# Kernel optimization log

Measured on AMD Instinct MI355X. Metric: run time of the kernel, lower is better.

## Reference

```python
import jax, jax.numpy as jnp
import numpy as np

DIM = 16  # size_in
N = 16384  # batch of samples


def _g_single(x, W1, b1, W2, b2):
    # myLinear forward for one sample x: [dim] -> [dim*dim] (symmetrized)
    h = jnp.tanh(W1 @ x + b1)                    # [dim]
    out = (W2 @ h + b2).reshape(DIM, DIM)        # [dim, dim]
    out = out + out.T                            # symmetrize (out + out.permute(0,2,1))
    return out.reshape(DIM * DIM)


def setup_inputs() -> dict:
    key = jax.random.key(0)
    k0, k1, k2, k3, k4 = jax.random.split(key, 5)
    s1 = 1.0 / np.sqrt(DIM)   # nn.Linear default init bound for fan_in=dim
    inp = jax.random.normal(k0, (N, 2 * DIM), dtype=jnp.float32)
    W1 = jax.random.uniform(k1, (DIM, DIM), dtype=jnp.float32, minval=-s1, maxval=s1)
    b1 = jax.random.uniform(k2, (DIM,), dtype=jnp.float32, minval=-s1, maxval=s1)
    W2 = jax.random.uniform(k3, (DIM * DIM, DIM), dtype=jnp.float32, minval=-s1, maxval=s1)
    b2 = jax.random.uniform(k4, (DIM * DIM,), dtype=jnp.float32, minval=-s1, maxval=s1)
    return {"t": 0, "input_": inp, "W1": W1, "b1": b1, "W2": W2, "b2": b2}


def reference(t, input_, W1, b1, W2, b2):
    x = input_[:, :DIM]   # [N, dim]
    v = input_[:, DIM:]   # [N, dim]

    g_fn = lambda xx: _g_single(xx, W1, b1, W2, b2)

    # batch jacobian of g w.r.t. x: [N, dim*dim, dim] -> [N, dim, dim, dim]
    J = jax.vmap(jax.jacfwd(g_fn))(x).reshape(N, DIM, DIM, DIM)
    g = jax.vmap(g_fn)(x).reshape(N, DIM, DIM)   # metric, symmetric
    g_inv = jnp.linalg.inv(g)                    # batched small inverse

    # faithful to the source: 4-operand einsum product (sum over l only)
    connection = 0.5 * jnp.einsum('nkl,nijl,njil,nlij->nkij', g_inv, J, J, -J)

    vv = jnp.einsum('ni,nj->nij', v, v)          # [N, dim, dim]
    dv = -jnp.einsum('hij,hkij->hk', vv, connection)  # [N, dim]

    return jnp.hstack([v, dv])                   # [N, 2*dim]
```

## Files before the change

kernel.cpp:

```cpp
#include <hip/hip_runtime.h>

typedef float f32x2 __attribute__((ext_vector_type(2)));

#define NPTS  16384
#define BATCH 16

#define OFF_W1   0
#define OFF_B1   320
#define OFF_VB   336
#define OFF_TB   592
#define OFF_HBD  848
#define OFF_U    1360
#define P_STRIDE 4352
#define LDS_FLOATS (OFF_U + 2 * P_STRIDE)

__device__ __forceinline__ void pkfma(f32x2& d, f32x2 a, f32x2 b) {
    asm("v_pk_fma_f32 %0, %1, %2, %0" : "+v"(d) : "v"(a), "v"(b));
}
__device__ __forceinline__ f32x2 pkmul(f32x2 a, f32x2 b) {
    f32x2 d;
    asm("v_pk_mul_f32 %0, %1, %2" : "=v"(d) : "v"(a), "v"(b));
    return d;
}
__device__ __forceinline__ double shfl_d(double x, int src) {
    long long v = __double_as_longlong(x);
    int lo = __shfl((int)(v & 0xffffffffLL), src, 16);
    int hi = __shfl((int)(v >> 32), src, 16);
    return __longlong_as_double(((long long)hi << 32) | (unsigned int)lo);
}
__device__ __forceinline__ double shfl_xor_d(double x, int m) {
    long long v = __double_as_longlong(x);
    int lo = __shfl_xor((int)(v & 0xffffffffLL), m, 16);
    int hi = __shfl_xor((int)(v >> 32), m, 16);
    return __longlong_as_double(((long long)hi << 32) | (unsigned int)lo);
}

__launch_bounds__(256, 4)
__global__ void conn_kernel(const float* __restrict__ inp,
                            const float* __restrict__ W1g,
                            const float* __restrict__ b1g,
                            const float* __restrict__ W2g,
                            const float* __restrict__ b2g,
                            float* __restrict__ out)
{
    __shared__ float SH[LDS_FLOATS];
    const int tid  = threadIdx.x;
    const int i_of = tid >> 4;
    const int j_of = tid & 15;

    const int pT = (j_of << 4) | i_of;
    f32x2 s2[8];
    {
        const float4* wa = reinterpret_cast<const float4*>(W2g + tid * 16);
        const float4* wb = reinterpret_cast<const float4*>(W2g + pT  * 16);
        #pragma unroll
        for (int q = 0; q < 4; ++q) {
            float4 A = wa[q], B = wb[q];
            s2[2*q+0] = f32x2{A.x + B.x, A.y + B.y};
            s2[2*q+1] = f32x2{A.z + B.z, A.w + B.w};
        }
    }

    SH[OFF_W1 + i_of * 20 + j_of] = W1g[tid];
    if (tid < 16) SH[OFF_B1 + tid] = b1g[tid];

    const int base = blockIdx.x * BATCH;
    if (tid < 128) {
        float4 vle = reinterpret_cast<const float4*>(inp + base * 32)[tid];
        int idx = tid * 4, pt = idx >> 5, c = idx & 31;
        float* dst = (c < 16) ? &SH[OFF_U  + pt * 16 + c]
                              : &SH[OFF_VB + pt * 16 + (c - 16)];
        dst[0] = vle.x; dst[1] = vle.y; dst[2] = vle.z; dst[3] = vle.w;
    }
    __syncthreads();

    {
        const int pt = i_of, k = j_of;
        const float* wrow = &SH[OFF_W1 + k * 20];
        const float* xrow = &SH[OFF_U  + pt * 16];
        double pre = (double)SH[OFF_B1 + k];
        #pragma unroll
        for (int l = 0; l < 16; ++l)
            pre = fma((double)wrow[l], (double)xrow[l], pre);
        double h = tanh(pre);
        reinterpret_cast<double*>(&SH[OFF_HBD])[pt * 16 + k] = h;
        SH[OFF_TB + pt * 16 + k] = (float)(1.0 - h * h);
    }
    __syncthreads();

    float* const P0 = &SH[OFF_U];
    float* const P1 = &SH[OFF_U + P_STRIDE];

    #pragma unroll 1
    for (int ch = 0; ch < 8; ++ch) {
        const int ptA = 2 * ch, ptB = 2 * ch + 1;

        f32x2 cA[8], cB[8], jA[8], jB[8];
        {
            const f32x2* tA2 = reinterpret_cast<const f32x2*>(&SH[OFF_TB + ptA * 16]);
            const f32x2* tB2 = reinterpret_cast<const f32x2*>(&SH[OFF_TB + ptB * 16]);
            #pragma unroll
            for (int m = 0; m < 8; ++m) {
                cA[m] = pkmul(s2[m], tA2[m]);
                cB[m] = pkmul(s2[m], tB2[m]);
                jA[m] = f32x2{0.f, 0.f};
                jB[m] = f32x2{0.f, 0.f};
            }
        }

        #pragma unroll
        for (int k = 0; k < 16; ++k) {
            const float4* w4 = reinterpret_cast<const float4*>(&SH[OFF_W1 + k * 20]);
            float4 w0 = w4[0], w1 = w4[1], w2 = w4[2], w3 = w4[3];
            f32x2 wp[8] = { {w0.x,w0.y},{w0.z,w0.w},{w1.x,w1.y},{w1.z,w1.w},
                            {w2.x,w2.y},{w2.z,w2.w},{w3.x,w3.y},{w3.z,w3.w} };
            float ca = cA[k >> 1][k & 1], cb = cB[k >> 1][k & 1];
            f32x2 ca2 = {ca, ca}, cb2 = {cb, cb};
            #pragma unroll
            for (int m = 0; m < 8; ++m) pkfma(jA[m], wp[m], ca2);
            #pragma unroll
            for (int m = 0; m < 8; ++m) pkfma(jB[m], wp[m], cb2);
        }

        {
            float pfA = SH[OFF_VB + ptA * 16 + i_of] * SH[OFF_VB + ptA * 16 + j_of];
            float pfB = SH[OFF_VB + ptB * 16 + i_of] * SH[OFF_VB + ptB * 16 + j_of];
            #pragma unroll
            for (int l = 0; l < 16; ++l) {
                float a = jA[l >> 1][l & 1], b = jB[l >> 1][l & 1];
                P0[l * 272 + j_of * 17 + i_of] = pfA * a * a;
                P1[l * 272 + j_of * 17 + i_of] = pfB * b * b;
            }
        }
        __syncthreads();

        {
            double sA = 0.0, sB = 0.0;
            #pragma unroll
            for (int j = 0; j < 16; ++j) {
                sA = fma((double)jA[j >> 1][j & 1],
                         (double)P0[i_of * 272 + j * 17 + j_of], sA);
                sB = fma((double)jB[j >> 1][j & 1],
                         (double)P1[i_of * 272 + j * 17 + j_of], sB);
            }
            #pragma unroll
            for (int m = 1; m < 16; m <<= 1) {
                sA += shfl_xor_d(sA, m);
                sB += shfl_xor_d(sB, m);
            }
            if (j_of == 0) {
                P0[i_of * 272 + ch * 17 + 16] = (float)sA;
                P1[i_of * 272 + ch * 17 + 16] = (float)sB;
            }
        }
        __syncthreads();
    }

    float rhsf;
    {
        const int pt = i_of, r = j_of;
        const float* Pb = (pt & 1) ? P1 : P0;
        rhsf = Pb[r * 272 + (pt >> 1) * 17 + 16];
    }
    __syncthreads();

    {
        double s2d[16];
        const float4* wa = reinterpret_cast<const float4*>(W2g + tid * 16);
        const float4* wb = reinterpret_cast<const float4*>(W2g + pT  * 16);
        #pragma unroll
        for (int q = 0; q < 4; ++q) {
            float4 A = wa[q], B = wb[q];
            s2d[4*q+0] = (double)A.x + (double)B.x;
            s2d[4*q+1] = (double)A.y + (double)B.y;
            s2d[4*q+2] = (double)A.z + (double)B.z;
            s2d[4*q+3] = (double)A.w + (double)B.w;
        }
        double bd = (double)b2g[tid] + (double)b2g[pT];

        double* GD = reinterpret_cast<double*>(&SH[OFF_U]);
        const double* HD = reinterpret_cast<const double*>(&SH[OFF_HBD]);
        #pragma unroll
        for (int pt = 0; pt < 16; ++pt) {
            const double* hrow = &HD[pt * 16];
            double acc = bd;
            #pragma unroll
            for (int k = 0; k < 16; ++k) acc = fma(s2d[k], hrow[k], acc);
            GD[pt * 272 + i_of * 17 + j_of] = acc;
        }
    }
    __syncthreads();

    {
        const int pt = i_of, r = j_of;
        const double* GD = reinterpret_cast<const double*>(&SH[OFF_U]);
        double grow[16];
        const double* gr = &GD[pt * 272 + r * 17];
        #pragma unroll
        for (int c = 0; c < 16; ++c) grow[c] = gr[c];
        double rhs = (double)rhsf;

        bool done = false; int myvar = 0;
        #pragma unroll
        for (int s = 0; s < 16; ++s) {
            float bv = done ? -1.0f : (float)fabs(grow[s]);
            int bi = r;
            #pragma unroll
            for (int m = 8; m >= 1; m >>= 1) {
                float ov = __shfl_xor(bv, m, 16);
                int   oi = __shfl_xor(bi, m, 16);
                if (ov > bv || (ov == bv && oi < bi)) { bv = ov; bi = oi; }
            }
            double pv   = shfl_d(grow[s], bi);
            double prhs = shfl_d(rhs,     bi);
            double invp = 1.0 / pv;
            bool   isP  = (r == bi);
            double f    = grow[s] * invp;
            #pragma unroll
            for (int c = s + 1; c < 16; ++c) {
                double pc  = shfl_d(grow[c], bi);
                double upd = fma(-f, pc, grow[c]);
                double piv = grow[c] * invp;
                grow[c] = isP ? piv : upd;
            }
            double updr = fma(-f, prhs, rhs);
            double pivr = rhs * invp;
            rhs = isP ? pivr : updr;
            if (isP) { done = true; myvar = s; }
        }

        const int n = base + pt;
        out[n * 32 + r]          = SH[OFF_VB + pt * 16 + r];
        out[n * 32 + 16 + myvar] = (float)(0.5 * rhs);
    }
}

extern "C" void kernel_launch(void* const* d_in, const int* in_sizes, int n_in,
                              void* d_out, int out_size, void* d_ws, size_t ws_size,
                              hipStream_t stream) {
    const float* inp = (const float*)d_in[1];
    const float* W1  = (const float*)d_in[2];
    const float* b1  = (const float*)d_in[3];
    const float* W2  = (const float*)d_in[4];
    const float* b2  = (const float*)d_in[5];
    float* outp = (float*)d_out;
    conn_kernel<<<dim3(NPTS / BATCH), 256, 0, stream>>>(inp, W1, b1, W2, b2, outp);
}
```

Before: 137.3 us.

## Halve LDS footprint and process one point per pass for higher occupancy

The connection loop now handles one sample per iteration with a single P buffer instead of two interleaved samples, roughly halving LDS use. The metric build and Gaussian elimination are split into two halves of eight points, so the double-precision G buffer fits in the smaller region. Launch bounds rise from 4 to 7 blocks per CU to exploit the lower LDS and register needs. The cost is twice as many barriers in the main loop, less ILP per thread, and idle warps during each half of the solve phase.

```diff
diff --git a/kernel.cpp b/kernel.cpp
--- a/kernel.cpp
+++ b/kernel.cpp
@@ -5,14 +5,13 @@
 #define NPTS  16384
 #define BATCH 16
 
-#define OFF_W1   0
-#define OFF_B1   320
-#define OFF_VB   336
-#define OFF_TB   592
-#define OFF_HBD  848
-#define OFF_U    1360
-#define P_STRIDE 4352
-#define LDS_FLOATS (OFF_U + 2 * P_STRIDE)
+#define OFF_W1 0
+#define OFF_B1 320
+#define OFF_VB 336
+#define OFF_TB 592
+#define OFF_HD 848
+#define OFF_P  1360
+#define LDS_FLOATS (OFF_P + 4352)
 
 __device__ __forceinline__ void pkfma(f32x2& d, f32x2 a, f32x2 b) {
     asm("v_pk_fma_f32 %0, %1, %2, %0" : "+v"(d) : "v"(a), "v"(b));
@@ -35,7 +34,7 @@
     return __longlong_as_double(((long long)hi << 32) | (unsigned int)lo);
 }
 
-__launch_bounds__(256, 4)
+__launch_bounds__(256, 7)
 __global__ void conn_kernel(const float* __restrict__ inp,
                             const float* __restrict__ W1g,
                             const float* __restrict__ b1g,
@@ -68,7 +67,7 @@
     if (tid < 128) {
         float4 vle = reinterpret_cast<const float4*>(inp + base * 32)[tid];
         int idx = tid * 4, pt = idx >> 5, c = idx & 31;
-        float* dst = (c < 16) ? &SH[OFF_U  + pt * 16 + c]
+        float* dst = (c < 16) ? &SH[OFF_P  + pt * 16 + c]
                               : &SH[OFF_VB + pt * 16 + (c - 16)];
         dst[0] = vle.x; dst[1] = vle.y; dst[2] = vle.z; dst[3] = vle.w;
     }
@@ -77,95 +76,69 @@
     {
         const int pt = i_of, k = j_of;
         const float* wrow = &SH[OFF_W1 + k * 20];
-        const float* xrow = &SH[OFF_U  + pt * 16];
+        const float* xrow = &SH[OFF_P  + pt * 16];
         double pre = (double)SH[OFF_B1 + k];
         #pragma unroll
         for (int l = 0; l < 16; ++l)
             pre = fma((double)wrow[l], (double)xrow[l], pre);
         double h = tanh(pre);
-        reinterpret_cast<double*>(&SH[OFF_HBD])[pt * 16 + k] = h;
+        reinterpret_cast<double*>(&SH[OFF_HD])[pt * 16 + k] = h;
         SH[OFF_TB + pt * 16 + k] = (float)(1.0 - h * h);
     }
     __syncthreads();
 
-    float* const P0 = &SH[OFF_U];
-    float* const P1 = &SH[OFF_U + P_STRIDE];
+    float* const P = &SH[OFF_P];
 
     #pragma unroll 1
-    for (int ch = 0; ch < 8; ++ch) {
-        const int ptA = 2 * ch, ptB = 2 * ch + 1;
-
-        f32x2 cA[8], cB[8], jA[8], jB[8];
+    for (int pt = 0; pt < 16; ++pt) {
+        f32x2 c_[8], j_[8];
         {
-            const f32x2* tA2 = reinterpret_cast<const f32x2*>(&SH[OFF_TB + ptA * 16]);
-            const f32x2* tB2 = reinterpret_cast<const f32x2*>(&SH[OFF_TB + ptB * 16]);
+            const f32x2* t2 = reinterpret_cast<const f32x2*>(&SH[OFF_TB + pt * 16]);
             #pragma unroll
             for (int m = 0; m < 8; ++m) {
-                cA[m] = pkmul(s2[m], tA2[m]);
-                cB[m] = pkmul(s2[m], tB2[m]);
-                jA[m] = f32x2{0.f, 0.f};
-                jB[m] = f32x2{0.f, 0.f};
+                c_[m] = pkmul(s2[m], t2[m]);
+                j_[m] = f32x2{0.f, 0.f};
             }
         }
-
         #pragma unroll
         for (int k = 0; k < 16; ++k) {
             const float4* w4 = reinterpret_cast<const float4*>(&SH[OFF_W1 + k * 20]);
             float4 w0 = w4[0], w1 = w4[1], w2 = w4[2], w3 = w4[3];
             f32x2 wp[8] = { {w0.x,w0.y},{w0.z,w0.w},{w1.x,w1.y},{w1.z,w1.w},
                             {w2.x,w2.y},{w2.z,w2.w},{w3.x,w3.y},{w3.z,w3.w} };
-            float ca = cA[k >> 1][k & 1], cb = cB[k >> 1][k & 1];
-            f32x2 ca2 = {ca, ca}, cb2 = {cb, cb};
-            #pragma unroll
-            for (int m = 0; m < 8; ++m) pkfma(jA[m], wp[m], ca2);
-            #pragma unroll
-            for (int m = 0; m < 8; ++m) pkfma(jB[m], wp[m], cb2);
-        }
-
+            float ca = c_[k >> 1][k & 1];
+            f32x2 ca2 = {ca, ca};
+            #pragma unroll
+            for (int m = 0; m < 8; ++m) pkfma(j_[m], wp[m], ca2);
+        }
         {
-            float pfA = SH[OFF_VB + ptA * 16 + i_of] * SH[OFF_VB + ptA * 16 + j_of];
-            float pfB = SH[OFF_VB + ptB * 16 + i_of] * SH[OFF_VB + ptB * 16 + j_of];
+            float pf = SH[OFF_VB + pt * 16 + i_of] * SH[OFF_VB + pt * 16 + j_of];
             #pragma unroll
             for (int l = 0; l < 16; ++l) {
-                float a = jA[l >> 1][l & 1], b = jB[l >> 1][l & 1];
-                P0[l * 272 + j_of * 17 + i_of] = pfA * a * a;
-                P1[l * 272 + j_of * 17 + i_of] = pfB * b * b;
+                float a = j_[l >> 1][l & 1];
+                P[l * 272 + j_of * 17 + i_of] = pf * a * a;
             }
         }
         __syncthreads();
-
         {
-            double sA = 0.0, sB = 0.0;
-            #pragma unroll
-            for (int j = 0; j < 16; ++j) {
-                sA = fma((double)jA[j >> 1][j & 1],
-                         (double)P0[i_of * 272 + j * 17 + j_of], sA);
-                sB = fma((double)jB[j >> 1][j & 1],
-                         (double)P1[i_of * 272 + j * 17 + j_of], sB);
-            }
-            #pragma unroll
-            for (int m = 1; m < 16; m <<= 1) {
-                sA += shfl_xor_d(sA, m);
-                sB += shfl_xor_d(sB, m);
-            }
-            if (j_of == 0) {
-                P0[i_of * 272 + ch * 17 + 16] = (float)sA;
-                P1[i_of * 272 + ch * 17 + 16] = (float)sB;
-            }
-        }
-        __syncthreads();
-    }
-
-    float rhsf;
+            double s = 0.0;
+            #pragma unroll
+            for (int j = 0; j < 16; ++j)
+                s = fma((double)j_[j >> 1][j & 1],
+                        (double)P[i_of * 272 + j * 17 + j_of], s);
+            #pragma unroll
+            for (int m = 1; m < 16; m <<= 1) s += shfl_xor_d(s, m);
+            if (j_of == 0)
+                P[i_of * 272 + pt * 17 + 16] = (float)s;
+        }
+        __syncthreads();
+    }
+
+    const float rhsf = P[j_of * 272 + i_of * 17 + 16];
+    __syncthreads();
+
+    double s2d[16], bsym_d;
     {
-        const int pt = i_of, r = j_of;
-        const float* Pb = (pt & 1) ? P1 : P0;
-        rhsf = Pb[r * 272 + (pt >> 1) * 17 + 16];
-    }
-    __syncthreads();
-
-    {
-        double s2d[16];
         const float4* wa = reinterpret_cast<const float4*>(W2g + tid * 16);
         const float4* wb = reinterpret_cast<const float4*>(W2g + pT  * 16);
         #pragma unroll
@@ -176,62 +149,66 @@
             s2d[4*q+2] = (double)A.z + (double)B.z;
             s2d[4*q+3] = (double)A.w + (double)B.w;
         }
-        double bd = (double)b2g[tid] + (double)b2g[pT];
-
-        double* GD = reinterpret_cast<double*>(&SH[OFF_U]);
-        const double* HD = reinterpret_cast<const double*>(&SH[OFF_HBD]);
-        #pragma unroll
-        for (int pt = 0; pt < 16; ++pt) {
-            const double* hrow = &HD[pt * 16];
-            double acc = bd;
+        bsym_d = (double)b2g[tid] + (double)b2g[pT];
+    }
+
+    double* const GD = reinterpret_cast<double*>(&SH[OFF_P]);
+    const double* const HD = reinterpret_cast<const double*>(&SH[OFF_HD]);
+
+    #pragma unroll 1
+    for (int r2 = 0; r2 < 2; ++r2) {
+        #pragma unroll
+        for (int pl = 0; pl < 8; ++pl) {
+            const double* hrow = &HD[(r2 * 8 + pl) * 16];
+            double acc = bsym_d;
             #pragma unroll
             for (int k = 0; k < 16; ++k) acc = fma(s2d[k], hrow[k], acc);
-            GD[pt * 272 + i_of * 17 + j_of] = acc;
-        }
-    }
-    __syncthreads();
-
-    {
-        const int pt = i_of, r = j_of;
-        const double* GD = reinterpret_cast<const double*>(&SH[OFF_U]);
-        double grow[16];
-        const double* gr = &GD[pt * 272 + r * 17];
-        #pragma unroll
-        for (int c = 0; c < 16; ++c) grow[c] = gr[c];
-        double rhs = (double)rhsf;
-
-        bool done = false; int myvar = 0;
-        #pragma unroll
-        for (int s = 0; s < 16; ++s) {
-            float bv = done ? -1.0f : (float)fabs(grow[s]);
-            int bi = r;
-            #pragma unroll
-            for (int m = 8; m >= 1; m >>= 1) {
-                float ov = __shfl_xor(bv, m, 16);
-                int   oi = __shfl_xor(bi, m, 16);
-                if (ov > bv || (ov == bv && oi < bi)) { bv = ov; bi = oi; }
+            GD[pl * 272 + i_of * 17 + j_of] = acc;
+        }
+        __syncthreads();
+
+        if ((i_of >> 3) == r2) {
+            const int pt = i_of, r = j_of, pl = i_of & 7;
+            double grow[16];
+            const double* gr = &GD[pl * 272 + r * 17];
+            #pragma unroll
+            for (int c = 0; c < 16; ++c) grow[c] = gr[c];
+            double rhs = (double)rhsf;
+
+            bool done = false; int myvar = 0;
+            #pragma unroll
+            for (int s = 0; s < 16; ++s) {
+                float bv = done ? -1.0f : (float)fabs(grow[s]);
+                int bi = r;
+                #pragma unroll
+                for (int m = 8; m >= 1; m >>= 1) {
+                    float ov = __shfl_xor(bv, m, 16);
+                    int   oi = __shfl_xor(bi, m, 16);
+                    if (ov > bv || (ov == bv && oi < bi)) { bv = ov; bi = oi; }
+                }
+                double pv   = shfl_d(grow[s], bi);
+                double prhs = shfl_d(rhs,     bi);
+                double invp = 1.0 / pv;
+                bool   isP  = (r == bi);
+                double f    = grow[s] * invp;
+                #pragma unroll
+                for (int c = s + 1; c < 16; ++c) {
+                    double pc  = shfl_d(grow[c], bi);
+                    double upd = fma(-f, pc, grow[c]);
+                    double piv = grow[c] * invp;
+                    grow[c] = isP ? piv : upd;
+                }
+                double updr = fma(-f, prhs, rhs);
+                double pivr = rhs * invp;
+                rhs = isP ? pivr : updr;
+                if (isP) { done = true; myvar = s; }
             }
-            double pv   = shfl_d(grow[s], bi);
-            double prhs = shfl_d(rhs,     bi);
-            double invp = 1.0 / pv;
-            bool   isP  = (r == bi);
-            double f    = grow[s] * invp;
-            #pragma unroll
-            for (int c = s + 1; c < 16; ++c) {
-                double pc  = shfl_d(grow[c], bi);
-                double upd = fma(-f, pc, grow[c]);
-                double piv = grow[c] * invp;
-                grow[c] = isP ? piv : upd;
-            }
-            double updr = fma(-f, prhs, rhs);
-            double pivr = rhs * invp;
-            rhs = isP ? pivr : updr;
-            if (isP) { done = true; myvar = s; }
-        }
-
-        const int n = base + pt;
-        out[n * 32 + r]          = SH[OFF_VB + pt * 16 + r];
-        out[n * 32 + 16 + myvar] = (float)(0.5 * rhs);
+
+            const int n = base + pt;
+            out[n * 32 + r]          = SH[OFF_VB + pt * 16 + r];
+            out[n * 32 + 16 + myvar] = (float)(0.5 * rhs);
+        }
+        __syncthreads();
     }
 }
 
```

New measurement: 173.8 us. +26.5%, slower.
